# Kernel tuning notes

Hardware: AMD Instinct MI355X
Metric: run time of the kernel (lower is better)

## Reference

```python
import jax, jax.numpy as jnp
import numpy as np

N_NODES = 50000
N_EDGES = 800000
HIDDEN = 128
N_GRAPHS = 128


def setup_inputs() -> dict:
    key = jax.random.key(0)
    ks = jax.random.split(key, 12)
    x = jax.random.normal(ks[0], (N_NODES, HIDDEN), dtype=jnp.float32)
    edge_index = jax.random.randint(ks[1], (2, N_EDGES), 0, N_NODES, dtype=jnp.int64)
    batch = jnp.sort(jax.random.randint(ks[2], (N_NODES,), 0, N_GRAPHS, dtype=jnp.int64))
    s = 1.0 / np.sqrt(HIDDEN)
    def lin(k):
        return jax.random.uniform(k, (HIDDEN, HIDDEN), jnp.float32, -s, s)
    return {
        "x": x,
        "edge_index": edge_index,
        "batch": batch,
        # layer 1 SAGEConv: lin_l (neighbor, with bias), lin_r (root, no bias)
        "wl1": lin(ks[3]), "b1": jax.random.uniform(ks[4], (HIDDEN,), jnp.float32, -s, s), "wr1": lin(ks[5]),
        # layer 2 SAGEConv
        "wl2": lin(ks[6]), "b2": jax.random.uniform(ks[7], (HIDDEN,), jnp.float32, -s, s), "wr2": lin(ks[8]),
        # classifier Linear
        "cw": lin(ks[9]), "cb": jax.random.uniform(ks[10], (HIDDEN,), jnp.float32, -s, s),
    }


def _sage_conv(x, src, dst, wl, b, wr, n_nodes):
    # mean aggregation of source features onto destination nodes
    agg = jax.ops.segment_sum(x[src], dst, num_segments=n_nodes)      # [N, H]
    deg = jax.ops.segment_sum(jnp.ones_like(dst, x.dtype), dst, num_segments=n_nodes)
    mean = agg / jnp.maximum(deg, 1.0)[:, None]
    # out = lin_l(mean) + lin_r(x); lin_l carries the bias (PyG convention)
    return mean @ wl.T + b + x @ wr.T


def reference(x, edge_index, batch, wl1, b1, wr1, wl2, b2, wr2, cw, cb):
    src, dst = edge_index[0], edge_index[1]
    n = x.shape[0]
    h = jax.nn.relu(_sage_conv(x, src, dst, wl1, b1, wr1, n))
    h = jax.nn.relu(_sage_conv(h, src, dst, wl2, b2, wr2, n))
    # global mean pool over graphs (dropout p=0.0 -> identity)
    gsum = jax.ops.segment_sum(h, batch, num_segments=N_GRAPHS)       # [G, H]
    gcnt = jax.ops.segment_sum(jnp.ones((n,), h.dtype), batch, num_segments=N_GRAPHS)
    pooled = gsum / jnp.maximum(gcnt, 1.0)[:, None]
    return pooled @ cw.T + cb
```

## Files before the change

kernel.cpp:

```cpp
#include <hip/hip_runtime.h>
#include <cstdint>
#include <cstddef>

#define HID 128
#define LDK 72
#define EPB 4096

typedef __attribute__((ext_vector_type(8))) short short8;
typedef __attribute__((ext_vector_type(4))) float floatx4;

__device__ __forceinline__ unsigned short f2bf(float f) {
  union { float f; uint32_t u; } c; c.f = f;
  uint32_t u = c.u;
  uint32_t r = (u + 0x7FFFu + ((u >> 16) & 1u)) >> 16;
  return (unsigned short)r;
}
__device__ __forceinline__ float bflo(uint32_t v) { return __uint_as_float(v << 16); }
__device__ __forceinline__ float bfhi(uint32_t v) { return __uint_as_float(v & 0xFFFF0000u); }
__device__ __forceinline__ float bf2f(unsigned short s) { return __uint_as_float(((uint32_t)s) << 16); }


__global__ __launch_bounds__(256) void k_zero_int(int* __restrict__ p, int n) {
  int i = blockIdx.x * 256 + threadIdx.x;
  if (i < n) p[i] = 0;
}


__global__ __launch_bounds__(256) void k_bucket_count(const int* __restrict__ dst,
                                                      int* __restrict__ bcnt, int E, int NB) {
  __shared__ int hist[256];
  const int t = threadIdx.x;
  hist[t] = 0;
  __syncthreads();
  const int per = (E + gridDim.x - 1) / gridDim.x;
  const int base = blockIdx.x * per;
  int end = base + per; if (end > E) end = E;
  for (int i = base + t; i < end; i += 256) atomicAdd(&hist[dst[i] >> 8], 1);
  __syncthreads();
  if (t < NB && hist[t]) atomicAdd(&bcnt[t], hist[t]);
}

__global__ __launch_bounds__(256) void k_scan196(const int* __restrict__ bcnt,
                                                 int* __restrict__ boff,
                                                 int* __restrict__ bcur, int NB) {
  __shared__ int s[256];
  int t = threadIdx.x;
  int v = (t < NB) ? bcnt[t] : 0;
  s[t] = v;
  __syncthreads();
  #pragma unroll
  for (int off = 1; off < 256; off <<= 1) {
    int add = (t >= off) ? s[t - off] : 0;
    __syncthreads();
    s[t] += add;
    __syncthreads();
  }
  if (t < NB) { int e = s[t] - v; boff[t] = e; bcur[t] = e; }
  if (t == 255) boff[NB] = s[255];
}

__global__ __launch_bounds__(256) void k_bucket(const int* __restrict__ src,
                                                const int* __restrict__ dst,
                                                int* __restrict__ bcur,
                                                uint32_t* __restrict__ ebuf,
                                                int E, int NB) {
  __shared__ int hist[256];
  __shared__ int lcur[256];
  const int t = threadIdx.x;
  const int base = blockIdx.x * EPB;
  hist[t] = 0;
  __syncthreads();

  uint32_t val[EPB / 256];
  int bk[EPB / 256];
  #pragma unroll
  for (int i = 0; i < EPB / 256; ++i) {
    int e = base + i * 256 + t;
    bk[i] = -1;
    if (e < E) {
      int d = dst[e];
      int s = src[e];
      bk[i] = d >> 8;
      val[i] = (uint32_t)s | ((uint32_t)(d & 255) << 16);
      atomicAdd(&hist[bk[i]], 1);
    }
  }
  __syncthreads();
  if (t < NB) {
    int c = hist[t];
    lcur[t] = c ? atomicAdd(&bcur[t], c) : 0;
  }
  __syncthreads();
  #pragma unroll
  for (int i = 0; i < EPB / 256; ++i) {
    if (bk[i] >= 0) {
      int pos = atomicAdd(&lcur[bk[i]], 1);
      ebuf[pos] = val[i];
    }
  }
}

__global__ __launch_bounds__(256) void k_bucket_fill2(const uint32_t* __restrict__ ebuf,
                                                      const int* __restrict__ boff,
                                                      int* __restrict__ rowptr,
                                                      unsigned short* __restrict__ csr16,
                                                      int N, int E, int NB) {
  __shared__ int hist[256];
  __shared__ int scan[256];
  const int b = blockIdx.x;
  const int t = threadIdx.x;
  hist[t] = 0;
  __syncthreads();
  const int lo = boff[b], hi = boff[b + 1];
  for (int i = lo + t; i < hi; i += 256) atomicAdd(&hist[ebuf[i] >> 16], 1);
  __syncthreads();
  int v = hist[t];
  scan[t] = v;
  __syncthreads();
  #pragma unroll
  for (int off = 1; off < 256; off <<= 1) {
    int add = (t >= off) ? scan[t - off] : 0;
    __syncthreads();
    scan[t] += add;
    __syncthreads();
  }
  int excl = scan[t] - v;
  int node = (b << 8) + t;
  if (node < N) rowptr[node] = lo + excl;
  if (b == NB - 1 && t == 0) rowptr[N] = E;
  hist[t] = lo + excl;
  __syncthreads();
  for (int i = lo + t; i < hi; i += 256) {
    uint32_t e = ebuf[i];
    int pos = atomicAdd(&hist[e >> 16], 1);
    csr16[pos] = (unsigned short)(e & 0xFFFFu);
  }
}


__global__ __launch_bounds__(256) void k_cast_bf16(const float* __restrict__ src,
                                                   unsigned short* __restrict__ dst, int n4) {
  int i = blockIdx.x * 256 + threadIdx.x;
  if (i < n4) {
    float4 v = ((const float4*)src)[i];
    uint32_t lo = (uint32_t)f2bf(v.x) | ((uint32_t)f2bf(v.y) << 16);
    uint32_t hi = (uint32_t)f2bf(v.z) | ((uint32_t)f2bf(v.w) << 16);
    ((uint2*)dst)[i] = make_uint2(lo, hi);
  }
}


__global__ __launch_bounds__(256) void k_aggregate(const unsigned short* __restrict__ feat,
                                                   const int* __restrict__ rowptr,
                                                   const unsigned short* __restrict__ csr16,
                                                   unsigned short* __restrict__ outmean, int N) {
  int wid = blockIdx.x * 4 + (threadIdx.x >> 6);
  int lane = threadIdx.x & 63;
  if (wid >= N) return;
  int start = rowptr[wid];
  int end   = rowptr[wid + 1];
  const int grp = lane >> 4;
  const int fl  = lane & 15;
  float a[8];
  #pragma unroll
  for (int i = 0; i < 8; ++i) a[i] = 0.f;

  for (int base = start; base < end; base += 64) {
    int m = end - base;
    if (m > 64) m = 64;
    int sidx = (base + lane < end) ? (int)csr16[base + lane] : 0;
    for (int j = 0; j < m; j += 8) {
      int j0 = j + grp, j1 = j + grp + 4;
      int s0 = __shfl(sidx, j0, 64);
      int s1 = __shfl(sidx, j1, 64);
      uint4 v0, v1;
      bool g0 = j0 < m, g1 = j1 < m;
      if (g0) v0 = *(const uint4*)(feat + (size_t)s0 * HID + fl * 8);
      if (g1) v1 = *(const uint4*)(feat + (size_t)s1 * HID + fl * 8);
      if (g0) {
        a[0] += bflo(v0.x); a[1] += bfhi(v0.x);
        a[2] += bflo(v0.y); a[3] += bfhi(v0.y);
        a[4] += bflo(v0.z); a[5] += bfhi(v0.z);
        a[6] += bflo(v0.w); a[7] += bfhi(v0.w);
      }
      if (g1) {
        a[0] += bflo(v1.x); a[1] += bfhi(v1.x);
        a[2] += bflo(v1.y); a[3] += bfhi(v1.y);
        a[4] += bflo(v1.z); a[5] += bfhi(v1.z);
        a[6] += bflo(v1.w); a[7] += bfhi(v1.w);
      }
    }
  }
  #pragma unroll
  for (int i = 0; i < 8; ++i) {
    a[i] += __shfl_xor(a[i], 16, 64);
    a[i] += __shfl_xor(a[i], 32, 64);
  }
  if (grp == 0) {
    int deg = end - start;
    float inv = 1.0f / (float)(deg > 1 ? deg : 1);
    uint4 o;
    o.x = (uint32_t)f2bf(a[0] * inv) | ((uint32_t)f2bf(a[1] * inv) << 16);
    o.y = (uint32_t)f2bf(a[2] * inv) | ((uint32_t)f2bf(a[3] * inv) << 16);
    o.z = (uint32_t)f2bf(a[4] * inv) | ((uint32_t)f2bf(a[5] * inv) << 16);
    o.w = (uint32_t)f2bf(a[6] * inv) | ((uint32_t)f2bf(a[7] * inv) << 16);
    *(uint4*)(outmean + (size_t)wid * HID + fl * 8) = o;
  }
}


__global__ __launch_bounds__(256, 2) void k_gemm_mfma(const unsigned short* __restrict__ A1,
                                                      const unsigned short* __restrict__ A2,
                                                      const float* __restrict__ WL,
                                                      const float* __restrict__ WR,
                                                      const float* __restrict__ bias,
                                                      unsigned short* __restrict__ outb,
                                                      const int* __restrict__ batch,
                                                      float* __restrict__ pooled,
                                                      int M, int relu) {
  __shared__ __align__(16) unsigned short sAB[2 * 128 * LDK];
  __shared__ int sB[128];
  unsigned short* sA = sAB;
  unsigned short* sW = sAB + 128 * LDK;
  const int t = threadIdx.x;
  const int lane = t & 63;
  const int wave = t >> 6;
  const int row0 = blockIdx.x * 128;
  const int mhalf = (wave & 1) * 64;
  const int nhalf = (wave >> 1) * 64;
  const int ml = lane & 15;
  const int q  = lane >> 4;

  floatx4 acc[4][4];
  #pragma unroll
  for (int a = 0; a < 4; ++a)
    #pragma unroll
    for (int b = 0; b < 4; ++b) acc[a][b] = (floatx4){0.f, 0.f, 0.f, 0.f};

  for (int stage = 0; stage < 4; ++stage) {
    const unsigned short* __restrict__ Asrc = (stage < 2) ? A1 : A2;
    const float* __restrict__ Wsrc = (stage < 2) ? WL : WR;
    const int k0g = (stage & 1) * 64;
    if (stage) __syncthreads();

    #pragma unroll
    for (int i = 0; i < 4; ++i) {
      int seg = t + i * 256;
      int r = seg >> 3, kc = (seg & 7) * 8;
      int gr = row0 + r;
      float4 v = make_float4(0.f, 0.f, 0.f, 0.f);
      if (gr < M) v = *(const float4*)(Asrc + (size_t)gr * HID + k0g + kc);
      *(float4*)&sA[r * LDK + kc] = v;
    }
    #pragma unroll
    for (int i = 0; i < 8; ++i) {
      int e = t + i * 256;
      int o = e >> 4, kc = (e & 15) * 4;
      float4 v = *(const float4*)(Wsrc + (size_t)o * HID + k0g + kc);
      uint32_t lo = (uint32_t)f2bf(v.x) | ((uint32_t)f2bf(v.y) << 16);
      uint32_t hi = (uint32_t)f2bf(v.z) | ((uint32_t)f2bf(v.w) << 16);
      *(uint2*)&sW[o * LDK + kc] = make_uint2(lo, hi);
    }
    __syncthreads();

    #pragma unroll
    for (int ks = 0; ks < 2; ++ks) {
      int kb = ks * 32 + q * 8;
      short8 af[4], bfr[4];
      #pragma unroll
      for (int mt = 0; mt < 4; ++mt)
        af[mt] = *(const short8*)&sA[(mhalf + mt * 16 + ml) * LDK + kb];
      #pragma unroll
      for (int nt = 0; nt < 4; ++nt)
        bfr[nt] = *(const short8*)&sW[(nhalf + nt * 16 + ml) * LDK + kb];
      #pragma unroll
      for (int mt = 0; mt < 4; ++mt)
        #pragma unroll
        for (int nt = 0; nt < 4; ++nt)
          acc[mt][nt] = __builtin_amdgcn_mfma_f32_16x16x32_bf16(af[mt], bfr[nt], acc[mt][nt], 0, 0, 0);
    }
  }

  if (pooled == nullptr) {
    #pragma unroll
    for (int nt = 0; nt < 4; ++nt) {
      int gcol = nhalf + nt * 16 + ml;
      float bv = bias[gcol];
      #pragma unroll
      for (int mt = 0; mt < 4; ++mt) {
        #pragma unroll
        for (int r = 0; r < 4; ++r) {
          int grow = row0 + mhalf + mt * 16 + q * 4 + r;
          if (grow < M) {
            float v = acc[mt][nt][r] + bv;
            if (relu) v = fmaxf(v, 0.f);
            outb[(size_t)grow * HID + gcol] = f2bf(v);
          }
        }
      }
    }
  } else {
    __syncthreads();
    unsigned short* sH = sAB;
    #pragma unroll
    for (int nt = 0; nt < 4; ++nt) {
      int gcol = nhalf + nt * 16 + ml;
      float bv = bias[gcol];
      #pragma unroll
      for (int mt = 0; mt < 4; ++mt) {
        #pragma unroll
        for (int r = 0; r < 4; ++r) {
          int lr = mhalf + mt * 16 + q * 4 + r;
          float v = acc[mt][nt][r] + bv;
          if (relu) v = fmaxf(v, 0.f);
          sH[lr * 128 + gcol] = f2bf(v);
        }
      }
    }
    if (t < 128) sB[t] = (row0 + t < M) ? batch[row0 + t] : -1;
    __syncthreads();
    const int f = t & 127, half = t >> 7;
    float pacc = 0.f;
    int curg = -1;
    for (int n = half; n < 128; n += 2) {
      int g = sB[n];
      if (g != curg) {
        if (curg >= 0) atomicAdd(&pooled[(size_t)curg * HID + f], pacc);
        curg = g; pacc = 0.f;
      }
      if (g >= 0) pacc += bf2f(sH[n * 128 + f]);
    }
    if (curg >= 0) atomicAdd(&pooled[(size_t)curg * HID + f], pacc);
  }
}


__device__ __forceinline__ int lower_bound_dev(const int* a, int n, int key) {
  int lo = 0, hi = n;
  while (lo < hi) {
    int mid = (lo + hi) >> 1;
    if (a[mid] < key) lo = mid + 1; else hi = mid;
  }
  return lo;
}

__global__ __launch_bounds__(256) void k_classify(const float* __restrict__ pooled,
                                                  const int* __restrict__ batch,
                                                  const float* __restrict__ cw,
                                                  const float* __restrict__ cb,
                                                  float* __restrict__ out, int N) {
  __shared__ int bnds[2];
  __shared__ float sp[128];
  __shared__ float part[2][128];
  int g = blockIdx.x;
  int t = threadIdx.x;
  if (t == 0) bnds[0] = lower_bound_dev(batch, N, g);
  if (t == 1) bnds[1] = lower_bound_dev(batch, N, g + 1);
  __syncthreads();
  int cnt = bnds[1] - bnds[0];
  float inv = 1.0f / (float)(cnt > 1 ? cnt : 1);
  if (t < 128) sp[t] = pooled[(size_t)g * HID + t] * inv;
  __syncthreads();
  int o = t & 127, kh = t >> 7;
  float a = 0.f;
  #pragma unroll 4
  for (int k = kh * 64; k < kh * 64 + 64; ++k) a += sp[k] * cw[(size_t)o * HID + k];
  part[kh][o] = a;
  __syncthreads();
  if (t < 128) out[(size_t)g * HID + t] = part[0][t] + part[1][t] + cb[t];
}


extern "C" void kernel_launch(void* const* d_in, const int* in_sizes, int n_in,
                              void* d_out, int out_size, void* d_ws, size_t ws_size,
                              hipStream_t stream) {
  const float* x     = (const float*)d_in[0];
  const int*   ei    = (const int*)d_in[1];
  const int*   batch = (const int*)d_in[2];
  const float* wl1   = (const float*)d_in[3];
  const float* b1    = (const float*)d_in[4];
  const float* wr1   = (const float*)d_in[5];
  const float* wl2   = (const float*)d_in[6];
  const float* b2    = (const float*)d_in[7];
  const float* wr2   = (const float*)d_in[8];
  const float* cw    = (const float*)d_in[9];
  const float* cb    = (const float*)d_in[10];
  float* out = (float*)d_out;

  const int N = in_sizes[0] / HID;
  const int E = in_sizes[1] / 2;
  const int G = out_size / HID;
  const int* src = ei;
  const int* dst = ei + E;

  char* w = (char*)d_ws;
  int*      bcnt   = (int*)(w);
  float*    pooled = (float*)(w + 1024);
  int*      boff   = (int*)(w + 66560);
  int*      bcur   = (int*)(w + 68608);
  int*      rowptr = (int*)(w + 69632);
  uint32_t* ebuf   = (uint32_t*)(w + 270336);
  unsigned short* csr16 = (unsigned short*)(w + 3470336);
  unsigned short* xb    = (unsigned short*)(w + 5070336);
  unsigned short* meanb = (unsigned short*)(w + 5070336 + 12800000);
  unsigned short* h1b   = (unsigned short*)(w + 5070336 + 25600000);
  unsigned short* h2_dummy = xb;

  const int NB = (N + 255) >> 8;
  const int aggBlocks  = (N + 3) / 4;
  const int gemmBlocks = (N + 127) / 128;
  const int castBlocks = (N * HID / 4 + 255) / 256;
  const int bktBlocks  = (E + EPB - 1) / EPB;
  const int zeroInts   = 66560 / 4;

  hipLaunchKernelGGL(k_zero_int,     dim3((zeroInts + 255) / 256), dim3(256), 0, stream, bcnt, zeroInts);
  hipLaunchKernelGGL(k_bucket_count, dim3(256), dim3(256), 0, stream, dst, bcnt, E, NB);
  hipLaunchKernelGGL(k_scan196,      dim3(1),   dim3(256), 0, stream, bcnt, boff, bcur, NB);
  hipLaunchKernelGGL(k_bucket,       dim3(bktBlocks), dim3(256), 0, stream, src, dst, bcur, ebuf, E, NB);
  hipLaunchKernelGGL(k_bucket_fill2, dim3(NB),  dim3(256), 0, stream, ebuf, boff, rowptr, csr16, N, E, NB);
  hipLaunchKernelGGL(k_cast_bf16,    dim3(castBlocks), dim3(256), 0, stream, x, xb, N * HID / 4);

  hipLaunchKernelGGL(k_aggregate, dim3(aggBlocks), dim3(256), 0, stream, xb, rowptr, csr16, meanb, N);
  hipLaunchKernelGGL(k_gemm_mfma, dim3(gemmBlocks), dim3(256), 0, stream, meanb, xb, wl1, wr1, b1, h1b,
                     (const int*)nullptr, (float*)nullptr, N, 1);
  hipLaunchKernelGGL(k_aggregate, dim3(aggBlocks), dim3(256), 0, stream, h1b, rowptr, csr16, meanb, N);
  hipLaunchKernelGGL(k_gemm_mfma, dim3(gemmBlocks), dim3(256), 0, stream, meanb, h1b, wl2, wr2, b2,
                     h2_dummy, batch, pooled, N, 1);
  hipLaunchKernelGGL(k_classify, dim3(G), dim3(256), 0, stream, pooled, batch, cw, cb, out, N);
}
```

Baseline: 242.8 us.

## Fuse neighbor aggregation into SAGE GEMM and use fixed-capacity edge buckets

Neighbor mean aggregation now runs inside the GEMM kernel, writing means straight into shared memory instead of a global intermediate. This removes a launch and a round trip per layer. Edge bucketing drops the count/scan prepass by giving each bucket a fixed CAP slot region and storing separate row begin/end arrays. In exchange the gather has fewer waves in flight per node, LDS use per block grows, and buckets assume at most CAP edges each.

```diff
diff --git a/kernel.cpp b/kernel.cpp
--- a/kernel.cpp
+++ b/kernel.cpp
@@ -4,7 +4,9 @@
 
 #define HID 128
 #define LDK 72
+#define LDM 136
 #define EPB 4096
+#define CAP 8192
 
 typedef __attribute__((ext_vector_type(8))) short short8;
 typedef __attribute__((ext_vector_type(4))) float floatx4;
@@ -19,45 +21,6 @@
 __device__ __forceinline__ float bfhi(uint32_t v) { return __uint_as_float(v & 0xFFFF0000u); }
 __device__ __forceinline__ float bf2f(unsigned short s) { return __uint_as_float(((uint32_t)s) << 16); }
 
-
-__global__ __launch_bounds__(256) void k_zero_int(int* __restrict__ p, int n) {
-  int i = blockIdx.x * 256 + threadIdx.x;
-  if (i < n) p[i] = 0;
-}
-
-
-__global__ __launch_bounds__(256) void k_bucket_count(const int* __restrict__ dst,
-                                                      int* __restrict__ bcnt, int E, int NB) {
-  __shared__ int hist[256];
-  const int t = threadIdx.x;
-  hist[t] = 0;
-  __syncthreads();
-  const int per = (E + gridDim.x - 1) / gridDim.x;
-  const int base = blockIdx.x * per;
-  int end = base + per; if (end > E) end = E;
-  for (int i = base + t; i < end; i += 256) atomicAdd(&hist[dst[i] >> 8], 1);
-  __syncthreads();
-  if (t < NB && hist[t]) atomicAdd(&bcnt[t], hist[t]);
-}
-
-__global__ __launch_bounds__(256) void k_scan196(const int* __restrict__ bcnt,
-                                                 int* __restrict__ boff,
-                                                 int* __restrict__ bcur, int NB) {
-  __shared__ int s[256];
-  int t = threadIdx.x;
-  int v = (t < NB) ? bcnt[t] : 0;
-  s[t] = v;
-  __syncthreads();
-  #pragma unroll
-  for (int off = 1; off < 256; off <<= 1) {
-    int add = (t >= off) ? s[t - off] : 0;
-    __syncthreads();
-    s[t] += add;
-    __syncthreads();
-  }
-  if (t < NB) { int e = s[t] - v; boff[t] = e; bcur[t] = e; }
-  if (t == 255) boff[NB] = s[255];
-}
 
 __global__ __launch_bounds__(256) void k_bucket(const int* __restrict__ src,
                                                 const int* __restrict__ dst,
@@ -94,24 +57,26 @@
   #pragma unroll
   for (int i = 0; i < EPB / 256; ++i) {
     if (bk[i] >= 0) {
-      int pos = atomicAdd(&lcur[bk[i]], 1);
+      int pos = bk[i] * CAP + atomicAdd(&lcur[bk[i]], 1);
       ebuf[pos] = val[i];
     }
   }
 }
 
 __global__ __launch_bounds__(256) void k_bucket_fill2(const uint32_t* __restrict__ ebuf,
-                                                      const int* __restrict__ boff,
-                                                      int* __restrict__ rowptr,
+                                                      const int* __restrict__ bcur,
+                                                      int* __restrict__ rowbeg,
+                                                      int* __restrict__ rowend,
                                                       unsigned short* __restrict__ csr16,
-                                                      int N, int E, int NB) {
+                                                      int N) {
   __shared__ int hist[256];
   __shared__ int scan[256];
   const int b = blockIdx.x;
   const int t = threadIdx.x;
   hist[t] = 0;
   __syncthreads();
-  const int lo = boff[b], hi = boff[b + 1];
+  const int lo = b * CAP;
+  const int hi = lo + bcur[b];
   for (int i = lo + t; i < hi; i += 256) atomicAdd(&hist[ebuf[i] >> 16], 1);
   __syncthreads();
   int v = hist[t];
@@ -126,8 +91,10 @@
   }
   int excl = scan[t] - v;
   int node = (b << 8) + t;
-  if (node < N) rowptr[node] = lo + excl;
-  if (b == NB - 1 && t == 0) rowptr[N] = E;
+  if (node < N) {
+    rowbeg[node] = lo + excl;
+    rowend[node] = lo + excl + v;
+  }
   hist[t] = lo + excl;
   __syncthreads();
   for (int i = lo + t; i < hi; i += 256) {
@@ -150,82 +117,81 @@
 }
 
 
-__global__ __launch_bounds__(256) void k_aggregate(const unsigned short* __restrict__ feat,
-                                                   const int* __restrict__ rowptr,
-                                                   const unsigned short* __restrict__ csr16,
-                                                   unsigned short* __restrict__ outmean, int N) {
-  int wid = blockIdx.x * 4 + (threadIdx.x >> 6);
-  int lane = threadIdx.x & 63;
-  if (wid >= N) return;
-  int start = rowptr[wid];
-  int end   = rowptr[wid + 1];
-  const int grp = lane >> 4;
-  const int fl  = lane & 15;
-  float a[8];
-  #pragma unroll
-  for (int i = 0; i < 8; ++i) a[i] = 0.f;
-
-  for (int base = start; base < end; base += 64) {
-    int m = end - base;
-    if (m > 64) m = 64;
-    int sidx = (base + lane < end) ? (int)csr16[base + lane] : 0;
-    for (int j = 0; j < m; j += 8) {
-      int j0 = j + grp, j1 = j + grp + 4;
-      int s0 = __shfl(sidx, j0, 64);
-      int s1 = __shfl(sidx, j1, 64);
-      uint4 v0, v1;
-      bool g0 = j0 < m, g1 = j1 < m;
-      if (g0) v0 = *(const uint4*)(feat + (size_t)s0 * HID + fl * 8);
-      if (g1) v1 = *(const uint4*)(feat + (size_t)s1 * HID + fl * 8);
-      if (g0) {
-        a[0] += bflo(v0.x); a[1] += bfhi(v0.x);
-        a[2] += bflo(v0.y); a[3] += bfhi(v0.y);
-        a[4] += bflo(v0.z); a[5] += bfhi(v0.z);
-        a[6] += bflo(v0.w); a[7] += bfhi(v0.w);
-      }
-      if (g1) {
-        a[0] += bflo(v1.x); a[1] += bfhi(v1.x);
-        a[2] += bflo(v1.y); a[3] += bfhi(v1.y);
-        a[4] += bflo(v1.z); a[5] += bfhi(v1.z);
-        a[6] += bflo(v1.w); a[7] += bfhi(v1.w);
-      }
-    }
-  }
-  #pragma unroll
-  for (int i = 0; i < 8; ++i) {
-    a[i] += __shfl_xor(a[i], 16, 64);
-    a[i] += __shfl_xor(a[i], 32, 64);
-  }
-  if (grp == 0) {
-    int deg = end - start;
-    float inv = 1.0f / (float)(deg > 1 ? deg : 1);
-    uint4 o;
-    o.x = (uint32_t)f2bf(a[0] * inv) | ((uint32_t)f2bf(a[1] * inv) << 16);
-    o.y = (uint32_t)f2bf(a[2] * inv) | ((uint32_t)f2bf(a[3] * inv) << 16);
-    o.z = (uint32_t)f2bf(a[4] * inv) | ((uint32_t)f2bf(a[5] * inv) << 16);
-    o.w = (uint32_t)f2bf(a[6] * inv) | ((uint32_t)f2bf(a[7] * inv) << 16);
-    *(uint4*)(outmean + (size_t)wid * HID + fl * 8) = o;
-  }
-}
-
-
-__global__ __launch_bounds__(256, 2) void k_gemm_mfma(const unsigned short* __restrict__ A1,
-                                                      const unsigned short* __restrict__ A2,
-                                                      const float* __restrict__ WL,
-                                                      const float* __restrict__ WR,
-                                                      const float* __restrict__ bias,
-                                                      unsigned short* __restrict__ outb,
-                                                      const int* __restrict__ batch,
-                                                      float* __restrict__ pooled,
-                                                      int M, int relu) {
-  __shared__ __align__(16) unsigned short sAB[2 * 128 * LDK];
+__global__ __launch_bounds__(256, 2) void k_sage_layer(const unsigned short* __restrict__ feat,
+                                                       const int* __restrict__ rowbeg,
+                                                       const int* __restrict__ rowend,
+                                                       const unsigned short* __restrict__ csr16,
+                                                       const float* __restrict__ WL,
+                                                       const float* __restrict__ WR,
+                                                       const float* __restrict__ bias,
+                                                       unsigned short* __restrict__ outb,
+                                                       const int* __restrict__ batch,
+                                                       float* __restrict__ pooled,
+                                                       int M, int relu) {
+  __shared__ __align__(16) unsigned short sMean[128 * LDM];
+  __shared__ __align__(16) unsigned short sA2[128 * LDK];
+  __shared__ __align__(16) unsigned short sW[128 * LDK];
   __shared__ int sB[128];
-  unsigned short* sA = sAB;
-  unsigned short* sW = sAB + 128 * LDK;
   const int t = threadIdx.x;
   const int lane = t & 63;
   const int wave = t >> 6;
   const int row0 = blockIdx.x * 128;
+
+  {
+    const int grp = lane >> 4;
+    const int fl  = lane & 15;
+    for (int nn = wave; nn < 128; nn += 4) {
+      int node = row0 + nn;
+      int start = 0, end = 0;
+      if (node < M) { start = rowbeg[node]; end = rowend[node]; }
+      float a[8];
+      #pragma unroll
+      for (int i = 0; i < 8; ++i) a[i] = 0.f;
+      for (int base = start; base < end; base += 64) {
+        int m = end - base;
+        if (m > 64) m = 64;
+        int sidx = (base + lane < end) ? (int)csr16[base + lane] : 0;
+        for (int j = 0; j < m; j += 8) {
+          int j0 = j + grp, j1 = j + grp + 4;
+          int s0 = __shfl(sidx, j0, 64);
+          int s1 = __shfl(sidx, j1, 64);
+          uint4 v0, v1;
+          bool g0 = j0 < m, g1 = j1 < m;
+          if (g0) v0 = *(const uint4*)(feat + (size_t)s0 * HID + fl * 8);
+          if (g1) v1 = *(const uint4*)(feat + (size_t)s1 * HID + fl * 8);
+          if (g0) {
+            a[0] += bflo(v0.x); a[1] += bfhi(v0.x);
+            a[2] += bflo(v0.y); a[3] += bfhi(v0.y);
+            a[4] += bflo(v0.z); a[5] += bfhi(v0.z);
+            a[6] += bflo(v0.w); a[7] += bfhi(v0.w);
+          }
+          if (g1) {
+            a[0] += bflo(v1.x); a[1] += bfhi(v1.x);
+            a[2] += bflo(v1.y); a[3] += bfhi(v1.y);
+            a[4] += bflo(v1.z); a[5] += bfhi(v1.z);
+            a[6] += bflo(v1.w); a[7] += bfhi(v1.w);
+          }
+        }
+      }
+      #pragma unroll
+      for (int i = 0; i < 8; ++i) {
+        a[i] += __shfl_xor(a[i], 16, 64);
+        a[i] += __shfl_xor(a[i], 32, 64);
+      }
+      if (grp == 0) {
+        int deg = end - start;
+        float inv = 1.0f / (float)(deg > 1 ? deg : 1);
+        uint4 o;
+        o.x = (uint32_t)f2bf(a[0] * inv) | ((uint32_t)f2bf(a[1] * inv) << 16);
+        o.y = (uint32_t)f2bf(a[2] * inv) | ((uint32_t)f2bf(a[3] * inv) << 16);
+        o.z = (uint32_t)f2bf(a[4] * inv) | ((uint32_t)f2bf(a[5] * inv) << 16);
+        o.w = (uint32_t)f2bf(a[6] * inv) | ((uint32_t)f2bf(a[7] * inv) << 16);
+        *(uint4*)&sMean[nn * LDM + fl * 8] = o;
+      }
+    }
+  }
+  __syncthreads();
+
   const int mhalf = (wave & 1) * 64;
   const int nhalf = (wave >> 1) * 64;
   const int ml = lane & 15;
@@ -238,20 +204,10 @@
     for (int b = 0; b < 4; ++b) acc[a][b] = (floatx4){0.f, 0.f, 0.f, 0.f};
 
   for (int stage = 0; stage < 4; ++stage) {
-    const unsigned short* __restrict__ Asrc = (stage < 2) ? A1 : A2;
     const float* __restrict__ Wsrc = (stage < 2) ? WL : WR;
     const int k0g = (stage & 1) * 64;
     if (stage) __syncthreads();
 
-    #pragma unroll
-    for (int i = 0; i < 4; ++i) {
-      int seg = t + i * 256;
-      int r = seg >> 3, kc = (seg & 7) * 8;
-      int gr = row0 + r;
-      float4 v = make_float4(0.f, 0.f, 0.f, 0.f);
-      if (gr < M) v = *(const float4*)(Asrc + (size_t)gr * HID + k0g + kc);
-      *(float4*)&sA[r * LDK + kc] = v;
-    }
     #pragma unroll
     for (int i = 0; i < 8; ++i) {
       int e = t + i * 256;
@@ -261,15 +217,32 @@
       uint32_t hi = (uint32_t)f2bf(v.z) | ((uint32_t)f2bf(v.w) << 16);
       *(uint2*)&sW[o * LDK + kc] = make_uint2(lo, hi);
     }
+    if (stage >= 2) {
+      #pragma unroll
+      for (int i = 0; i < 4; ++i) {
+        int seg = t + i * 256;
+        int r = seg >> 3, kc = (seg & 7) * 8;
+        int gr = row0 + r;
+        float4 v = make_float4(0.f, 0.f, 0.f, 0.f);
+        if (gr < M) v = *(const float4*)(feat + (size_t)gr * HID + k0g + kc);
+        *(float4*)&sA2[r * LDK + kc] = v;
+      }
+    }
     __syncthreads();
 
     #pragma unroll
     for (int ks = 0; ks < 2; ++ks) {
       int kb = ks * 32 + q * 8;
       short8 af[4], bfr[4];
-      #pragma unroll
-      for (int mt = 0; mt < 4; ++mt)
-        af[mt] = *(const short8*)&sA[(mhalf + mt * 16 + ml) * LDK + kb];
+      if (stage < 2) {
+        #pragma unroll
+        for (int mt = 0; mt < 4; ++mt)
+          af[mt] = *(const short8*)&sMean[(mhalf + mt * 16 + ml) * LDM + k0g + kb];
+      } else {
+        #pragma unroll
+        for (int mt = 0; mt < 4; ++mt)
+          af[mt] = *(const short8*)&sA2[(mhalf + mt * 16 + ml) * LDK + kb];
+      }
       #pragma unroll
       for (int nt = 0; nt < 4; ++nt)
         bfr[nt] = *(const short8*)&sW[(nhalf + nt * 16 + ml) * LDK + kb];
@@ -301,7 +274,7 @@
     }
   } else {
     __syncthreads();
-    unsigned short* sH = sAB;
+    unsigned short* sH = sMean;
     #pragma unroll
     for (int nt = 0; nt < 4; ++nt) {
       int gcol = nhalf + nt * 16 + ml;
@@ -394,37 +367,31 @@
   const int* dst = ei + E;
 
   char* w = (char*)d_ws;
-  int*      bcnt   = (int*)(w);
+  int*      bcur   = (int*)(w);
   float*    pooled = (float*)(w + 1024);
-  int*      boff   = (int*)(w + 66560);
-  int*      bcur   = (int*)(w + 68608);
-  int*      rowptr = (int*)(w + 69632);
-  uint32_t* ebuf   = (uint32_t*)(w + 270336);
-  unsigned short* csr16 = (unsigned short*)(w + 3470336);
-  unsigned short* xb    = (unsigned short*)(w + 5070336);
-  unsigned short* meanb = (unsigned short*)(w + 5070336 + 12800000);
-  unsigned short* h1b   = (unsigned short*)(w + 5070336 + 25600000);
-  unsigned short* h2_dummy = xb;
+  int*      rowbeg = (int*)(w + 66560);
+  int*      rowend = (int*)(w + 266560);
+  uint32_t* ebuf   = (uint32_t*)(w + 466944);
+  unsigned short* csr16 = (unsigned short*)(w + 6889472);
+  unsigned short* xb    = (unsigned short*)(w + 10100736);
+  unsigned short* h1b   = (unsigned short*)(w + 10100736 + 12800000);
 
   const int NB = (N + 255) >> 8;
-  const int aggBlocks  = (N + 3) / 4;
-  const int gemmBlocks = (N + 127) / 128;
+  const int sageBlocks = (N + 127) / 128;
   const int castBlocks = (N * HID / 4 + 255) / 256;
   const int bktBlocks  = (E + EPB - 1) / EPB;
-  const int zeroInts   = 66560 / 4;
-
-  hipLaunchKernelGGL(k_zero_int,     dim3((zeroInts + 255) / 256), dim3(256), 0, stream, bcnt, zeroInts);
-  hipLaunchKernelGGL(k_bucket_count, dim3(256), dim3(256), 0, stream, dst, bcnt, E, NB);
-  hipLaunchKernelGGL(k_scan196,      dim3(1),   dim3(256), 0, stream, bcnt, boff, bcur, NB);
+
+  hipMemsetAsync(w, 0, 66560, stream);
+
   hipLaunchKernelGGL(k_bucket,       dim3(bktBlocks), dim3(256), 0, stream, src, dst, bcur, ebuf, E, NB);
-  hipLaunchKernelGGL(k_bucket_fill2, dim3(NB),  dim3(256), 0, stream, ebuf, boff, rowptr, csr16, N, E, NB);
+  hipLaunchKernelGGL(k_bucket_fill2, dim3(NB),  dim3(256), 0, stream, ebuf, bcur, rowbeg, rowend, csr16, N);
   hipLaunchKernelGGL(k_cast_bf16,    dim3(castBlocks), dim3(256), 0, stream, x, xb, N * HID / 4);
 
-  hipLaunchKernelGGL(k_aggregate, dim3(aggBlocks), dim3(256), 0, stream, xb, rowptr, csr16, meanb, N);
-  hipLaunchKernelGGL(k_gemm_mfma, dim3(gemmBlocks), dim3(256), 0, stream, meanb, xb, wl1, wr1, b1, h1b,
+  hipLaunchKernelGGL(k_sage_layer, dim3(sageBlocks), dim3(256), 0, stream,
+                     xb, rowbeg, rowend, csr16, wl1, wr1, b1, h1b,
                      (const int*)nullptr, (float*)nullptr, N, 1);
-  hipLaunchKernelGGL(k_aggregate, dim3(aggBlocks), dim3(256), 0, stream, h1b, rowptr, csr16, meanb, N);
-  hipLaunchKernelGGL(k_gemm_mfma, dim3(gemmBlocks), dim3(256), 0, stream, meanb, h1b, wl2, wr2, b2,
-                     h2_dummy, batch, pooled, N, 1);
+  hipLaunchKernelGGL(k_sage_layer, dim3(sageBlocks), dim3(256), 0, stream,
+                     h1b, rowbeg, rowend, csr16, wl2, wr2, b2,
+                     (unsigned short*)nullptr, batch, pooled, N, 1);
   hipLaunchKernelGGL(k_classify, dim3(G), dim3(256), 0, stream, pooled, batch, cw, cb, out, N);
 }
```

Result: slower. 335.0 us (+38.0%).
